# Kernel tuning notes

Hardware: AMD Instinct MI355X
Metric: run time of the kernel (lower is better)

The kernel has to match this reference:

```python
import jax, jax.numpy as jnp
import numpy as np

NUM_STEPS = 64  # num_steps from init
DROP_P = 0.5


def _lstm_cell(x, h, c, W_ih, W_hh, b_ih, b_hh):
    # PyTorch LSTMCell: gates ordered i, f, g, o
    g = x @ W_ih.T + b_ih + h @ W_hh.T + b_hh
    i, f, gg, o = jnp.split(g, 4, axis=-1)
    c2 = jax.nn.sigmoid(f) * c + jax.nn.sigmoid(i) * jnp.tanh(gg)
    h2 = jax.nn.sigmoid(o) * jnp.tanh(c2)
    return h2, c2


def setup_inputs() -> dict:
    key = jax.random.key(0)
    ks = jax.random.split(key, 12)
    s = 0.02
    return {
        "xs": jax.random.normal(ks[0], (128, 128, 512), jnp.float32),
        "W_ih0": jax.random.normal(ks[1], (4096, 512), jnp.float32) * s,
        "W_hh0": jax.random.normal(ks[2], (4096, 1024), jnp.float32) * s,
        "b_ih0": jax.random.normal(ks[3], (4096,), jnp.float32) * s,
        "b_hh0": jax.random.normal(ks[4], (4096,), jnp.float32) * s,
        "W_ih1": jax.random.normal(ks[5], (4096, 1024), jnp.float32) * s,
        "W_hh1": jax.random.normal(ks[6], (4096, 1024), jnp.float32) * s,
        "b_ih1": jax.random.normal(ks[7], (4096,), jnp.float32) * s,
        "b_hh1": jax.random.normal(ks[8], (4096,), jnp.float32) * s,
        "W_cls": jax.random.normal(ks[9], (1000, 1024), jnp.float32) * s,
        "b_cls": jax.random.normal(ks[10], (1000,), jnp.float32) * s,
        "drop_u": jax.random.uniform(ks[11], (128, 1024), jnp.float32),
    }


def reference(xs, W_ih0, W_hh0, b_ih0, b_hh0, W_ih1, W_hh1, b_ih1, b_hh1,
              W_cls, b_cls, drop_u):
    B, T, D = xs.shape
    start = T - NUM_STEPS - 9  # forward reads xs[:, -num_steps-9+t, :]
    seq = jnp.transpose(xs[:, start:start + NUM_STEPS, :], (1, 0, 2))  # [S,B,D]
    H0, H1 = W_hh0.shape[1], W_hh1.shape[1]
    init = (jnp.zeros((B, H0), xs.dtype), jnp.zeros((B, H0), xs.dtype),
            jnp.zeros((B, H1), xs.dtype), jnp.zeros((B, H1), xs.dtype))

    def step(carry, x):
        h0, c0, h1, c1 = carry
        h0, c0 = _lstm_cell(x, h0, c0, W_ih0, W_hh0, b_ih0, b_hh0)
        h1, c1 = _lstm_cell(h0, h1, c1, W_ih1, W_hh1, b_ih1, b_hh1)
        return (h0, c0, h1, c1), None

    (h0, c0, h1, c1), _ = jax.lax.scan(step, init, seq)
    # F.dropout(p=0.5) with a deterministic mask derived from drop_u
    keep = (drop_u > DROP_P).astype(xs.dtype)
    x = h1 * keep / (1.0 - DROP_P)
    return x @ W_cls.T + b_cls
```

## Files before the change

kernel.cpp:

```cpp
#include <hip/hip_runtime.h>
#include <hip/hip_bf16.h>
#include <hip/hip_cooperative_groups.h>


typedef __attribute__((ext_vector_type(8))) short s8v;
typedef __attribute__((ext_vector_type(4))) float f4v;
typedef unsigned short bfu;

#define BATCH 128
#define HID   1024
#define NSTEP 64
#define TDIM  128
#define DDIM  512
#define TSTART 55
#define HSLOT 131072

__device__ __forceinline__ bfu f2bf(float f) {
    union { float f; unsigned int u; } v; v.f = f;
    unsigned int r = (v.u + 0x7FFFu + ((v.u >> 16) & 1u)) >> 16;
    return (bfu)r;
}
__device__ __forceinline__ float sigm(float x) {
    return 1.f / (1.f + __expf(-x));
}

__device__ __forceinline__ void load8_sc(const bfu* p, s8v (&o)[8]) {
    const bfu* p2 = p + 2048;
    asm volatile(
        "global_load_dwordx4 %0, %[a0], off sc0 sc1\n\t"
        "global_load_dwordx4 %1, %[a0], off offset:1024 sc0 sc1\n\t"
        "global_load_dwordx4 %2, %[a0], off offset:2048 sc0 sc1\n\t"
        "global_load_dwordx4 %3, %[a0], off offset:3072 sc0 sc1\n\t"
        "global_load_dwordx4 %4, %[a1], off sc0 sc1\n\t"
        "global_load_dwordx4 %5, %[a1], off offset:1024 sc0 sc1\n\t"
        "global_load_dwordx4 %6, %[a1], off offset:2048 sc0 sc1\n\t"
        "global_load_dwordx4 %7, %[a1], off offset:3072 sc0 sc1\n\t"
        "s_waitcnt vmcnt(0)"
        : "=&v"(o[0]), "=&v"(o[1]), "=&v"(o[2]), "=&v"(o[3]),
          "=&v"(o[4]), "=&v"(o[5]), "=&v"(o[6]), "=&v"(o[7])
        : [a0]"v"(p), [a1]"v"(p2)
        : "memory");
}

__global__ void prep_kernel(
    const float* __restrict__ xs,
    const float* __restrict__ Wih0, const float* __restrict__ Whh0,
    const float* __restrict__ Wih1, const float* __restrict__ Whh1,
    const float* __restrict__ Wcls,
    const float* __restrict__ bih0, const float* __restrict__ bhh0,
    const float* __restrict__ bih1, const float* __restrict__ bhh1,
    bfu* __restrict__ xbf, bfu* __restrict__ wih0b, bfu* __restrict__ whh0b,
    bfu* __restrict__ wih1b, bfu* __restrict__ whh1b, bfu* __restrict__ wclsb,
    float* __restrict__ bias0, float* __restrict__ bias1,
    bfu* __restrict__ h0ring, bfu* __restrict__ h1ring, int* __restrict__ flags)
{
    const size_t NX  = (size_t)NSTEP * BATCH * DDIM;
    const size_t E1  = NX  + (size_t)4096 * 512;
    const size_t E2  = E1  + (size_t)4096 * 1024;
    const size_t E3  = E2  + (size_t)4096 * 1024;
    const size_t E4  = E3  + (size_t)4096 * 1024;
    const size_t E5  = E4  + (size_t)1000 * 1024;
    const size_t E6  = E5  + 4096;
    const size_t E7  = E6  + 4096;
    const size_t E8  = E7  + HSLOT;
    const size_t E9  = E8  + HSLOT;
    const size_t E10 = E9  + 1024;

    size_t stride = (size_t)gridDim.x * blockDim.x;
    for (size_t i = (size_t)blockIdx.x * blockDim.x + threadIdx.x; i < E10; i += stride) {
        if (i < NX) {
            size_t t   = i >> 16;
            int    rem = (int)(i & 65535);
            int chunk = rem >> 9;
            int le    = rem & 511;
            int l = le >> 3, e = le & 7;
            int m  = chunk >> 4;
            int kk = chunk & 15;
            int row = m * 16 + (l & 15);
            int k   = kk * 32 + (l >> 4) * 8 + e;
            xbf[i] = f2bf(xs[(size_t)row * (TDIM * DDIM) + (TSTART + t) * DDIM + k]);
        } else if (i < E1) { size_t j = i - NX;  wih0b[j] = f2bf(Wih0[j]); }
        else if (i < E2)   { size_t j = i - E1;  whh0b[j] = f2bf(Whh0[j]); }
        else if (i < E3)   { size_t j = i - E2;  wih1b[j] = f2bf(Wih1[j]); }
        else if (i < E4)   { size_t j = i - E3;  whh1b[j] = f2bf(Whh1[j]); }
        else if (i < E5)   { size_t j = i - E4;  wclsb[j] = f2bf(Wcls[j]); }
        else if (i < E6)   { size_t j = i - E5;  bias0[j] = bih0[j] + bhh0[j]; }
        else if (i < E7)   { size_t j = i - E6;  bias1[j] = bih1[j] + bhh1[j]; }
        else if (i < E8)   { h0ring[i - E7] = 0; }
        else if (i < E9)   { h1ring[i - E8] = 0; }
        else               { flags[i - E9] = 0; }
    }
}

template<bool SC1, int CH1>
__device__ __forceinline__ void layer_step(
    const bfu* __restrict__ A1, const bfu* __restrict__ A2,
    const bfu* __restrict__ wlds, float (*eps)[33],
    bfu* __restrict__ h_out, float* __restrict__ h_out_f32,
    int tid, int n0, const float (&bg)[8], float& cA, float& cB)
{
    const int l  = tid & 63;
    const int w  = tid >> 6;
    const int lr = l & 15;
    const int kg = l >> 4;

    f4v acc0 = {0.f, 0.f, 0.f, 0.f};
    f4v acc1 = {0.f, 0.f, 0.f, 0.f};

    {
        const bfu* ap  = A1 + (size_t)(w * CH1) * 512 + l * 8;
        const bfu* b0p = wlds + l * 8;
        const bfu* b1p = wlds + (size_t)CH1 * 512 + l * 8;
        if constexpr (SC1) {
            #pragma unroll
            for (int g = 0; g < CH1 / 8; ++g) {
                s8v o[8];
                load8_sc(ap, o); ap += 8 * 512;
                #pragma unroll
                for (int c = 0; c < 8; ++c) {
                    s8v b0 = *(const s8v*)b0p; b0p += 512;
                    s8v b1 = *(const s8v*)b1p; b1p += 512;
                    acc0 = __builtin_amdgcn_mfma_f32_16x16x32_bf16(o[c], b0, acc0, 0, 0, 0);
                    acc1 = __builtin_amdgcn_mfma_f32_16x16x32_bf16(o[c], b1, acc1, 0, 0, 0);
                }
            }
        } else {
            #pragma unroll 8
            for (int kk = 0; kk < CH1; ++kk) {
                s8v a  = *(const s8v*)ap;  ap  += 512;
                s8v b0 = *(const s8v*)b0p; b0p += 512;
                s8v b1 = *(const s8v*)b1p; b1p += 512;
                acc0 = __builtin_amdgcn_mfma_f32_16x16x32_bf16(a, b0, acc0, 0, 0, 0);
                acc1 = __builtin_amdgcn_mfma_f32_16x16x32_bf16(a, b1, acc1, 0, 0, 0);
            }
        }
    }
    {
        const bfu* ap  = A2 + (size_t)(w * 32) * 512 + l * 8;
        const bfu* b0p = wlds + (size_t)(2 * CH1) * 512 + l * 8;
        const bfu* b1p = wlds + (size_t)(2 * CH1 + 32) * 512 + l * 8;
        #pragma unroll
        for (int g = 0; g < 4; ++g) {
            s8v o[8];
            load8_sc(ap, o); ap += 8 * 512;
            #pragma unroll
            for (int c = 0; c < 8; ++c) {
                s8v b0 = *(const s8v*)b0p; b0p += 512;
                s8v b1 = *(const s8v*)b1p; b1p += 512;
                acc0 = __builtin_amdgcn_mfma_f32_16x16x32_bf16(o[c], b0, acc0, 0, 0, 0);
                acc1 = __builtin_amdgcn_mfma_f32_16x16x32_bf16(o[c], b1, acc1, 0, 0, 0);
            }
        }
    }

    {
        const int rbase = w * 16 + kg * 4;
        #pragma unroll
        for (int r = 0; r < 4; ++r) {
            eps[rbase + r][lr]      = acc0[r];
            eps[rbase + r][16 + lr] = acc1[r];
        }
    }
    __syncthreads();

    {
        const int row = tid >> 2;
        const int up  = tid & 3;
        const int e0  = 2 * up;
        const int ne  = n0 + e0;
        float gi0 = eps[row][e0]          + bg[0];
        float gi1 = eps[row][e0 + 1]      + bg[1];
        float gf0 = eps[row][8 + e0]      + bg[2];
        float gf1 = eps[row][8 + e0 + 1]  + bg[3];
        float gg0 = eps[row][16 + e0]     + bg[4];
        float gg1 = eps[row][16 + e0 + 1] + bg[5];
        float go0 = eps[row][24 + e0]     + bg[6];
        float go1 = eps[row][24 + e0 + 1] + bg[7];
        float cn0 = sigm(gf0) * cA + sigm(gi0) * tanhf(gg0);
        float cn1 = sigm(gf1) * cB + sigm(gi1) * tanhf(gg1);
        cA = cn0; cB = cn1;
        float hn0 = sigm(go0) * tanhf(cn0);
        float hn1 = sigm(go1) * tanhf(cn1);
        const int idx = ((row >> 4) * 32 + (ne >> 5)) * 512
                      + (((ne >> 3) & 3) * 16 + (row & 15)) * 8 + (ne & 7);
        unsigned int pk = (unsigned int)f2bf(hn0) | ((unsigned int)f2bf(hn1) << 16);
        __hip_atomic_store((unsigned int*)(h_out + idx), pk,
                           __ATOMIC_RELAXED, __HIP_MEMORY_SCOPE_AGENT);
        if (h_out_f32) {
            h_out_f32[(size_t)row * HID + ne]     = hn0;
            h_out_f32[(size_t)row * HID + ne + 1] = hn1;
        }
    }
    asm volatile("s_waitcnt vmcnt(0)" ::: "memory");
    __syncthreads();
}

__global__ __launch_bounds__(512)
void persist_kernel(
    const bfu* __restrict__ xbf,
    const bfu* __restrict__ wih0, const bfu* __restrict__ whh0,
    const bfu* __restrict__ wih1, const bfu* __restrict__ whh1,
    const float* __restrict__ bias0, const float* __restrict__ bias1,
    bfu* __restrict__ h0ring, bfu* __restrict__ h1ring,
    float* __restrict__ h1f, int* __restrict__ flags)
{
    __shared__ bfu   wlds[65536];
    __shared__ float eps[128][33];

    const int tid  = threadIdx.x;
    const int role = blockIdx.x & 1;
    const int n0   = (blockIdx.x >> 1) * 8;

    int* h0done = flags;
    int* h1done = flags + 64;
    int* h0rel  = flags + 128;

    const bfu*   W1   = role ? wih1 : wih0;
    const bfu*   W2   = role ? whh1 : whh0;
    const float* bias = role ? bias1 : bias0;
    const int    K1   = role ? 1024 : 512;
    const int    CH1  = K1 >> 5;

    {
        const int units = (2 * CH1 + 64) * 64;
        for (int u0 = tid; u0 < units; u0 += 512) {
            const int c = u0 >> 6, l = u0 & 63;
            const int lr = l & 15, kg = l >> 4;
            const bfu* Wsrc; int K, nt, kk;
            if (c < 2 * CH1) { Wsrc = W1; K = K1;   nt = c / CH1; kk = c % CH1; }
            else { const int c2 = c - 2 * CH1; Wsrc = W2; K = 1024; nt = c2 >> 5; kk = c2 & 31; }
            const int cl = nt * 16 + lr;
            const int j  = (cl >> 3) * HID + n0 + (cl & 7);
            s8v v = *(const s8v*)(Wsrc + (size_t)j * K + kk * 32 + kg * 8);
            *(s8v*)(wlds + (size_t)c * 512 + l * 8) = v;
        }
    }
    __syncthreads();

    float bg[8];
    {
        const int ne = n0 + 2 * (tid & 3);
        bg[0] = bias[ne];             bg[1] = bias[ne + 1];
        bg[2] = bias[HID + ne];       bg[3] = bias[HID + ne + 1];
        bg[4] = bias[2 * HID + ne];   bg[5] = bias[2 * HID + ne + 1];
        bg[6] = bias[3 * HID + ne];   bg[7] = bias[3 * HID + ne + 1];
    }
    float cA = 0.f, cB = 0.f;

    if (role == 0) {
        for (int t = 0; t < NSTEP; ++t) {
            if (tid == 0) {
                if (t > 0)
                    while (__hip_atomic_load(&h0done[t - 1], __ATOMIC_RELAXED,
                                             __HIP_MEMORY_SCOPE_AGENT) < 128)
                        __builtin_amdgcn_s_sleep(1);
                if (t >= 16)
                    while (__hip_atomic_load(&h0rel[t - 16], __ATOMIC_RELAXED,
                                             __HIP_MEMORY_SCOPE_AGENT) < 128)
                        __builtin_amdgcn_s_sleep(1);
            }
            __syncthreads();
            const bfu* h0prev = h0ring + (size_t)(t & 15) * HSLOT;
            bfu*       h0cur  = h0ring + (size_t)((t + 1) & 15) * HSLOT;
            layer_step<false, 16>(xbf + (size_t)t * 65536, h0prev, wlds, eps,
                                  h0cur, nullptr, tid, n0, bg, cA, cB);
            if (tid == 0)
                __hip_atomic_fetch_add(&h0done[t], 1, __ATOMIC_RELAXED,
                                       __HIP_MEMORY_SCOPE_AGENT);
        }
    } else {
        for (int t = 0; t < NSTEP; ++t) {
            if (tid == 0) {
                while (__hip_atomic_load(&h0done[t], __ATOMIC_RELAXED,
                                         __HIP_MEMORY_SCOPE_AGENT) < 128)
                    __builtin_amdgcn_s_sleep(1);
                if (t > 0)
                    while (__hip_atomic_load(&h1done[t - 1], __ATOMIC_RELAXED,
                                             __HIP_MEMORY_SCOPE_AGENT) < 128)
                        __builtin_amdgcn_s_sleep(1);
            }
            __syncthreads();
            const bfu* h0t    = h0ring + (size_t)((t + 1) & 15) * HSLOT;
            const bfu* h1prev = h1ring + (size_t)(t & 3) * HSLOT;
            bfu*       h1cur  = h1ring + (size_t)((t + 1) & 3) * HSLOT;
            layer_step<true, 32>(h0t, h1prev, wlds, eps,
                                 h1cur, (t == NSTEP - 1) ? h1f : nullptr,
                                 tid, n0, bg, cA, cB);
            if (tid == 0) {
                __hip_atomic_fetch_add(&h1done[t], 1, __ATOMIC_RELAXED,
                                       __HIP_MEMORY_SCOPE_AGENT);
                __hip_atomic_fetch_add(&h0rel[t], 1, __ATOMIC_RELAXED,
                                       __HIP_MEMORY_SCOPE_AGENT);
            }
        }
    }
}

__global__ __launch_bounds__(512)
void cls_kernel(const float* __restrict__ h1f, const float* __restrict__ du,
                const bfu* __restrict__ Wc, const float* __restrict__ bc,
                float* __restrict__ out)
{
    const int tid = threadIdx.x;
    const int l   = tid & 63;
    const int w   = tid >> 6;
    const int lr  = l & 15;
    const int kg  = l >> 4;
    const int j   = blockIdx.x * 16 + lr;
    const int jW  = (j < 1000) ? j : 999;

    f4v acc = {0.f, 0.f, 0.f, 0.f};
    const float* hp = h1f + (size_t)(w * 16 + lr) * HID + kg * 8;
    const float* dp = du  + (size_t)(w * 16 + lr) * HID + kg * 8;
    const bfu*   bp = Wc  + (size_t)jW * HID + kg * 8;
    #pragma unroll 4
    for (int kk = 0; kk < HID; kk += 32) {
        f4v h0v = *(const f4v*)hp;
        f4v h1v = *(const f4v*)(hp + 4);
        f4v d0v = *(const f4v*)dp;
        f4v d1v = *(const f4v*)(dp + 4);
        s8v a;
        #pragma unroll
        for (int e = 0; e < 4; ++e) {
            a[e]     = (short)f2bf(d0v[e] > 0.5f ? h0v[e] * 2.f : 0.f);
            a[4 + e] = (short)f2bf(d1v[e] > 0.5f ? h1v[e] * 2.f : 0.f);
        }
        s8v b = *(const s8v*)bp;
        acc = __builtin_amdgcn_mfma_f32_16x16x32_bf16(a, b, acc, 0, 0, 0);
        hp += 32; dp += 32; bp += 32;
    }
    if (j < 1000) {
        const float bj = bc[j];
        const int rbase = w * 16 + kg * 4;
        #pragma unroll
        for (int r = 0; r < 4; ++r)
            out[(size_t)(rbase + r) * 1000 + j] = acc[r] + bj;
    }
}

extern "C" void kernel_launch(void* const* d_in, const int* in_sizes, int n_in,
                              void* d_out, int out_size, void* d_ws, size_t ws_size,
                              hipStream_t stream)
{
    const float* xs   = (const float*)d_in[0];
    const float* Wih0 = (const float*)d_in[1];
    const float* Whh0 = (const float*)d_in[2];
    const float* bih0 = (const float*)d_in[3];
    const float* bhh0 = (const float*)d_in[4];
    const float* Wih1 = (const float*)d_in[5];
    const float* Whh1 = (const float*)d_in[6];
    const float* bih1 = (const float*)d_in[7];
    const float* bhh1 = (const float*)d_in[8];
    const float* Wcls = (const float*)d_in[9];
    const float* bcls = (const float*)d_in[10];
    const float* du   = (const float*)d_in[11];
    float* out = (float*)d_out;

    char* p = (char*)d_ws;
    auto alloc = [&](size_t bytes) {
        char* r = p; p += (bytes + 255) & ~(size_t)255; return r;
    };
    bfu*   xbf   = (bfu*)  alloc((size_t)NSTEP * BATCH * DDIM * 2);
    bfu*   wih0b = (bfu*)  alloc((size_t)4096 * 512 * 2);
    bfu*   whh0b = (bfu*)  alloc((size_t)4096 * 1024 * 2);
    bfu*   wih1b = (bfu*)  alloc((size_t)4096 * 1024 * 2);
    bfu*   whh1b = (bfu*)  alloc((size_t)4096 * 1024 * 2);
    bfu*   wclsb = (bfu*)  alloc((size_t)1000 * 1024 * 2);
    float* bias0 = (float*)alloc(4096 * 4);
    float* bias1 = (float*)alloc(4096 * 4);
    bfu*   h0ring = (bfu*) alloc((size_t)16 * HSLOT * 2);
    bfu*   h1ring = (bfu*) alloc((size_t)4 * HSLOT * 2);
    float* h1f    = (float*)alloc((size_t)BATCH * HID * 4);
    int*   flags  = (int*) alloc(1024 * 4);
    (void)ws_size; (void)in_sizes; (void)n_in; (void)out_size;

    prep_kernel<<<2048, 256, 0, stream>>>(
        xs, Wih0, Whh0, Wih1, Whh1, Wcls, bih0, bhh0, bih1, bhh1,
        xbf, wih0b, whh0b, wih1b, whh1b, wclsb, bias0, bias1,
        h0ring, h1ring, flags);

    {
        void* args[] = {
            (void*)&xbf, (void*)&wih0b, (void*)&whh0b, (void*)&wih1b,
            (void*)&whh1b, (void*)&bias0, (void*)&bias1,
            (void*)&h0ring, (void*)&h1ring, (void*)&h1f, (void*)&flags
        };
        hipLaunchCooperativeKernel((const void*)persist_kernel,
                                   dim3(256), dim3(512), args, 0, stream);
    }

    cls_kernel<<<63, 512, 0, stream>>>(h1f, du, wclsb, bcls, out);
}
```

Measured before the change: 827.4 us.

## Split LSTM persistent kernel into four GEMM roles with partial-sum handoff

Splits each LSTM layer's work across four block roles: the input projection for layer 0, the recurrent projection for layer 0, the input projection for layer 1, and the recurrent projection for layer 1. The input-projection roles write fp32 partial gate sums that the recurrent roles add before the LSTM epilogue. This takes the input GEMMs off the serial recurrence path and lets them run ahead. It also moves from 16x16x32 to 32x32x16 MFMA tiles with a matching xbf and weight layout, shrinks the h0 ring, and replaces the cooperative launch with a plain launch. The cost is extra global partial-sum traffic and many more flag spin-waits. It also depends on all 256 blocks being co-resident without the cooperative-launch guarantee.

```diff
diff --git a/kernel.cpp b/kernel.cpp
--- a/kernel.cpp
+++ b/kernel.cpp
@@ -1,10 +1,10 @@
 #include <hip/hip_runtime.h>
 #include <hip/hip_bf16.h>
-#include <hip/hip_cooperative_groups.h>
-
-
-typedef __attribute__((ext_vector_type(8))) short s8v;
-typedef __attribute__((ext_vector_type(4))) float f4v;
+
+
+typedef __attribute__((ext_vector_type(8)))  short s8v;
+typedef __attribute__((ext_vector_type(4)))  float f4v;
+typedef __attribute__((ext_vector_type(16))) float f16v;
 typedef unsigned short bfu;
 
 #define BATCH 128
@@ -15,6 +15,13 @@
 #define TSTART 55
 #define HSLOT 131072
 
+#define F_H0D(t)  ((t) * 16)
+#define F_H1D(t)  (1024 + (t) * 16)
+#define F_PCN(t)  (2048 + (t) * 16)
+#define F_XD(t,i) (3072 + (t) * 64 + (i))
+#define F_PD(t,i) (7168 + (t) * 64 + (i))
+#define NFLAGS    11264
+
 __device__ __forceinline__ bfu f2bf(float f) {
     union { float f; unsigned int u; } v; v.f = f;
     unsigned int r = (v.u + 0x7FFFu + ((v.u >> 16) & 1u)) >> 16;
@@ -22,6 +29,12 @@
 }
 __device__ __forceinline__ float sigm(float x) {
     return 1.f / (1.f + __expf(-x));
+}
+__device__ __forceinline__ f16v zero16() {
+    f16v a;
+    #pragma unroll
+    for (int r = 0; r < 16; ++r) a[r] = 0.f;
+    return a;
 }
 
 __device__ __forceinline__ void load8_sc(const bfu* p, s8v (&o)[8]) {
@@ -42,6 +55,35 @@
         : "memory");
 }
 
+__device__ __forceinline__ void store16_sc(float* p, const f16v& a) {
+    f4v v0 = {a[0], a[1], a[2], a[3]},   v1 = {a[4], a[5], a[6], a[7]};
+    f4v v2 = {a[8], a[9], a[10], a[11]}, v3 = {a[12], a[13], a[14], a[15]};
+    asm volatile(
+        "global_store_dwordx4 %0, %1, off sc0 sc1\n\t"
+        "global_store_dwordx4 %0, %2, off offset:16 sc0 sc1\n\t"
+        "global_store_dwordx4 %0, %3, off offset:32 sc0 sc1\n\t"
+        "global_store_dwordx4 %0, %4, off offset:48 sc0 sc1"
+        :: "v"(p), "v"(v0), "v"(v1), "v"(v2), "v"(v3)
+        : "memory");
+}
+
+__device__ __forceinline__ void addpart_sc(const float* p, f16v& acc) {
+    f4v v0, v1, v2, v3;
+    asm volatile(
+        "global_load_dwordx4 %0, %[ad], off sc0 sc1\n\t"
+        "global_load_dwordx4 %1, %[ad], off offset:16 sc0 sc1\n\t"
+        "global_load_dwordx4 %2, %[ad], off offset:32 sc0 sc1\n\t"
+        "global_load_dwordx4 %3, %[ad], off offset:48 sc0 sc1\n\t"
+        "s_waitcnt vmcnt(0)"
+        : "=&v"(v0), "=&v"(v1), "=&v"(v2), "=&v"(v3)
+        : [ad]"v"(p) : "memory");
+    #pragma unroll
+    for (int r = 0; r < 4; ++r) {
+        acc[r] += v0[r]; acc[4 + r] += v1[r];
+        acc[8 + r] += v2[r]; acc[12 + r] += v3[r];
+    }
+}
+
 __global__ void prep_kernel(
     const float* __restrict__ xs,
     const float* __restrict__ Wih0, const float* __restrict__ Whh0,
@@ -64,7 +106,7 @@
     const size_t E7  = E6  + 4096;
     const size_t E8  = E7  + HSLOT;
     const size_t E9  = E8  + HSLOT;
-    const size_t E10 = E9  + 1024;
+    const size_t E10 = E9  + NFLAGS;
 
     size_t stride = (size_t)gridDim.x * blockDim.x;
     for (size_t i = (size_t)blockIdx.x * blockDim.x + threadIdx.x; i < E10; i += stride) {
@@ -72,12 +114,11 @@
             size_t t   = i >> 16;
             int    rem = (int)(i & 65535);
             int chunk = rem >> 9;
-            int le    = rem & 511;
-            int l = le >> 3, e = le & 7;
-            int m  = chunk >> 4;
-            int kk = chunk & 15;
-            int row = m * 16 + (l & 15);
-            int k   = kk * 32 + (l >> 4) * 8 + e;
+            int l = (rem >> 3) & 63, e = rem & 7;
+            int m  = chunk >> 5;
+            int ks = chunk & 31;
+            int row = m * 32 + (l & 31);
+            int k   = ks * 16 + (l >> 5) * 8 + e;
             xbf[i] = f2bf(xs[(size_t)row * (TDIM * DDIM) + (TSTART + t) * DDIM + k]);
         } else if (i < E1) { size_t j = i - NX;  wih0b[j] = f2bf(Wih0[j]); }
         else if (i < E2)   { size_t j = i - E1;  whh0b[j] = f2bf(Whh0[j]); }
@@ -92,106 +133,85 @@
     }
 }
 
-template<bool SC1, int CH1>
-__device__ __forceinline__ void layer_step(
-    const bfu* __restrict__ A1, const bfu* __restrict__ A2,
-    const bfu* __restrict__ wlds, float (*eps)[33],
-    bfu* __restrict__ h_out, float* __restrict__ h_out_f32,
-    int tid, int n0, const float (&bg)[8], float& cA, float& cB)
-{
-    const int l  = tid & 63;
-    const int w  = tid >> 6;
-    const int lr = l & 15;
-    const int kg = l >> 4;
-
-    f4v acc0 = {0.f, 0.f, 0.f, 0.f};
-    f4v acc1 = {0.f, 0.f, 0.f, 0.f};
-
-    {
-        const bfu* ap  = A1 + (size_t)(w * CH1) * 512 + l * 8;
-        const bfu* b0p = wlds + l * 8;
-        const bfu* b1p = wlds + (size_t)CH1 * 512 + l * 8;
-        if constexpr (SC1) {
+template<bool SC, int KS>
+__device__ __forceinline__ void gemm32(const bfu* __restrict__ Abase,
+                                       const bfu* __restrict__ bbase,
+                                       f16v& acc, int m, int l)
+{
+    const bfu* ap = Abase + (size_t)(m * KS) * 512 + l * 8;
+    const bfu* bp = bbase + l * 8;
+    #pragma unroll
+    for (int g = 0; g < KS / 8; ++g) {
+        s8v o[8];
+        if constexpr (SC) {
+            load8_sc(ap, o);
+        } else {
             #pragma unroll
-            for (int g = 0; g < CH1 / 8; ++g) {
-                s8v o[8];
-                load8_sc(ap, o); ap += 8 * 512;
-                #pragma unroll
-                for (int c = 0; c < 8; ++c) {
-                    s8v b0 = *(const s8v*)b0p; b0p += 512;
-                    s8v b1 = *(const s8v*)b1p; b1p += 512;
-                    acc0 = __builtin_amdgcn_mfma_f32_16x16x32_bf16(o[c], b0, acc0, 0, 0, 0);
-                    acc1 = __builtin_amdgcn_mfma_f32_16x16x32_bf16(o[c], b1, acc1, 0, 0, 0);
-                }
+            for (int c = 0; c < 8; ++c) o[c] = *(const s8v*)(ap + c * 512);
+        }
+        ap += 8 * 512;
+        #pragma unroll
+        for (int c = 0; c < 8; ++c) {
+            s8v b = *(const s8v*)bp; bp += 512;
+            acc = __builtin_amdgcn_mfma_f32_32x32x16_bf16(o[c], b, acc, 0, 0, 0);
+        }
+    }
+}
+
+__device__ __forceinline__ void lstm_epi32(
+    f16v& acc, float (*eps)[66], int tid, int n0,
+    const float* bgq, float* cst, bfu* __restrict__ h_out,
+    float* __restrict__ h1f_opt)
+{
+    const int l = tid & 63, w = tid >> 6;
+    const int m = w >> 1, nt = w & 1, hi = l >> 5, cc = l & 31;
+    const int row64 = tid >> 3, up = tid & 7;
+    const int u0 = 2 * up;
+    const int cb = ((u0 >> 3) * 32) + (u0 & 7);
+    const int k = n0 + u0;
+
+    #pragma unroll
+    for (int h = 0; h < 2; ++h) {
+        if ((m >> 1) == h) {
+            #pragma unroll
+            for (int r = 0; r < 16; ++r)
+                eps[(m & 1) * 32 + (r & 3) + 8 * (r >> 2) + 4 * hi][nt * 32 + cc] = acc[r];
+        }
+        __syncthreads();
+        {
+            const int row = h * 64 + row64;
+            float gi0 = eps[row64][cb]      + bgq[0];
+            float gi1 = eps[row64][cb + 1]  + bgq[1];
+            float gf0 = eps[row64][cb + 8]  + bgq[2];
+            float gf1 = eps[row64][cb + 9]  + bgq[3];
+            float gg0 = eps[row64][cb + 16] + bgq[4];
+            float gg1 = eps[row64][cb + 17] + bgq[5];
+            float go0 = eps[row64][cb + 24] + bgq[6];
+            float go1 = eps[row64][cb + 25] + bgq[7];
+            float cn0 = sigm(gf0) * cst[h * 2]     + sigm(gi0) * tanhf(gg0);
+            float cn1 = sigm(gf1) * cst[h * 2 + 1] + sigm(gi1) * tanhf(gg1);
+            cst[h * 2] = cn0; cst[h * 2 + 1] = cn1;
+            float hn0 = sigm(go0) * tanhf(cn0);
+            float hn1 = sigm(go1) * tanhf(cn1);
+            const int chunk = (row >> 5) * 64 + (k >> 4);
+            const int lp = ((k >> 3) & 1) * 32 + (row & 31);
+            const int elem = chunk * 512 + lp * 8 + (k & 7);
+            unsigned int pk = (unsigned int)f2bf(hn0) | ((unsigned int)f2bf(hn1) << 16);
+            __hip_atomic_store((unsigned int*)(h_out + elem), pk,
+                               __ATOMIC_RELAXED, __HIP_MEMORY_SCOPE_AGENT);
+            if (h1f_opt) {
+                h1f_opt[(size_t)row * HID + k]     = hn0;
+                h1f_opt[(size_t)row * HID + k + 1] = hn1;
             }
-        } else {
-            #pragma unroll 8
-            for (int kk = 0; kk < CH1; ++kk) {
-                s8v a  = *(const s8v*)ap;  ap  += 512;
-                s8v b0 = *(const s8v*)b0p; b0p += 512;
-                s8v b1 = *(const s8v*)b1p; b1p += 512;
-                acc0 = __builtin_amdgcn_mfma_f32_16x16x32_bf16(a, b0, acc0, 0, 0, 0);
-                acc1 = __builtin_amdgcn_mfma_f32_16x16x32_bf16(a, b1, acc1, 0, 0, 0);
-            }
-        }
-    }
-    {
-        const bfu* ap  = A2 + (size_t)(w * 32) * 512 + l * 8;
-        const bfu* b0p = wlds + (size_t)(2 * CH1) * 512 + l * 8;
-        const bfu* b1p = wlds + (size_t)(2 * CH1 + 32) * 512 + l * 8;
-        #pragma unroll
-        for (int g = 0; g < 4; ++g) {
-            s8v o[8];
-            load8_sc(ap, o); ap += 8 * 512;
-            #pragma unroll
-            for (int c = 0; c < 8; ++c) {
-                s8v b0 = *(const s8v*)b0p; b0p += 512;
-                s8v b1 = *(const s8v*)b1p; b1p += 512;
-                acc0 = __builtin_amdgcn_mfma_f32_16x16x32_bf16(o[c], b0, acc0, 0, 0, 0);
-                acc1 = __builtin_amdgcn_mfma_f32_16x16x32_bf16(o[c], b1, acc1, 0, 0, 0);
-            }
-        }
-    }
-
-    {
-        const int rbase = w * 16 + kg * 4;
-        #pragma unroll
-        for (int r = 0; r < 4; ++r) {
-            eps[rbase + r][lr]      = acc0[r];
-            eps[rbase + r][16 + lr] = acc1[r];
-        }
-    }
-    __syncthreads();
-
-    {
-        const int row = tid >> 2;
-        const int up  = tid & 3;
-        const int e0  = 2 * up;
-        const int ne  = n0 + e0;
-        float gi0 = eps[row][e0]          + bg[0];
-        float gi1 = eps[row][e0 + 1]      + bg[1];
-        float gf0 = eps[row][8 + e0]      + bg[2];
-        float gf1 = eps[row][8 + e0 + 1]  + bg[3];
-        float gg0 = eps[row][16 + e0]     + bg[4];
-        float gg1 = eps[row][16 + e0 + 1] + bg[5];
-        float go0 = eps[row][24 + e0]     + bg[6];
-        float go1 = eps[row][24 + e0 + 1] + bg[7];
-        float cn0 = sigm(gf0) * cA + sigm(gi0) * tanhf(gg0);
-        float cn1 = sigm(gf1) * cB + sigm(gi1) * tanhf(gg1);
-        cA = cn0; cB = cn1;
-        float hn0 = sigm(go0) * tanhf(cn0);
-        float hn1 = sigm(go1) * tanhf(cn1);
-        const int idx = ((row >> 4) * 32 + (ne >> 5)) * 512
-                      + (((ne >> 3) & 3) * 16 + (row & 15)) * 8 + (ne & 7);
-        unsigned int pk = (unsigned int)f2bf(hn0) | ((unsigned int)f2bf(hn1) << 16);
-        __hip_atomic_store((unsigned int*)(h_out + idx), pk,
-                           __ATOMIC_RELAXED, __HIP_MEMORY_SCOPE_AGENT);
-        if (h_out_f32) {
-            h_out_f32[(size_t)row * HID + ne]     = hn0;
-            h_out_f32[(size_t)row * HID + ne + 1] = hn1;
-        }
-    }
-    asm volatile("s_waitcnt vmcnt(0)" ::: "memory");
+        }
+        __syncthreads();
+    }
+}
+
+__device__ __forceinline__ void waitflag(int* p, int target, int tid) {
+    if (tid == 0)
+        while (__hip_atomic_load(p, __ATOMIC_RELAXED, __HIP_MEMORY_SCOPE_AGENT) < target)
+            __builtin_amdgcn_s_sleep(1);
     __syncthreads();
 }
 
@@ -202,96 +222,104 @@
     const bfu* __restrict__ wih1, const bfu* __restrict__ whh1,
     const float* __restrict__ bias0, const float* __restrict__ bias1,
     bfu* __restrict__ h0ring, bfu* __restrict__ h1ring,
-    float* __restrict__ h1f, int* __restrict__ flags)
+    float* __restrict__ xpart, float* __restrict__ ppart,
+    float* __restrict__ h1f, int* __restrict__ F)
 {
     __shared__ bfu   wlds[65536];
-    __shared__ float eps[128][33];
+    __shared__ float eps[64][66];
 
     const int tid  = threadIdx.x;
-    const int role = blockIdx.x & 1;
-    const int n0   = (blockIdx.x >> 1) * 8;
-
-    int* h0done = flags;
-    int* h1done = flags + 64;
-    int* h0rel  = flags + 128;
-
-    const bfu*   W1   = role ? wih1 : wih0;
-    const bfu*   W2   = role ? whh1 : whh0;
-    const float* bias = role ? bias1 : bias0;
-    const int    K1   = role ? 1024 : 512;
-    const int    CH1  = K1 >> 5;
-
-    {
-        const int units = (2 * CH1 + 64) * 64;
-        for (int u0 = tid; u0 < units; u0 += 512) {
-            const int c = u0 >> 6, l = u0 & 63;
-            const int lr = l & 15, kg = l >> 4;
-            const bfu* Wsrc; int K, nt, kk;
-            if (c < 2 * CH1) { Wsrc = W1; K = K1;   nt = c / CH1; kk = c % CH1; }
-            else { const int c2 = c - 2 * CH1; Wsrc = W2; K = 1024; nt = c2 >> 5; kk = c2 & 31; }
-            const int cl = nt * 16 + lr;
-            const int j  = (cl >> 3) * HID + n0 + (cl & 7);
-            s8v v = *(const s8v*)(Wsrc + (size_t)j * K + kk * 32 + kg * 8);
-            *(s8v*)(wlds + (size_t)c * 512 + l * 8) = v;
-        }
+    const int role = blockIdx.x & 3;
+    const int i    = blockIdx.x >> 2;
+    const int n0   = i * 16;
+    const int l = tid & 63, w = tid >> 6;
+    const int m = w >> 1, nt = w & 1;
+
+    const bfu* Wsrc; const float* bias = nullptr; int K;
+    if      (role == 0) { Wsrc = wih0; K = 512; }
+    else if (role == 1) { Wsrc = whh0; K = 1024; bias = bias0; }
+    else if (role == 2) { Wsrc = wih1; K = 1024; }
+    else                { Wsrc = whh1; K = 1024; bias = bias1; }
+    const int KSr = K >> 4;
+    const int ksh = (K == 512) ? 5 : 6;
+
+    for (int u = tid; u < 2 * KSr * 64; u += 512) {
+        int c = u >> 6, ll = u & 63;
+        int ntc = c >> ksh, ks = c & (KSr - 1);
+        int j  = ((ll >> 3) & 3) * 1024 + n0 + ntc * 8 + (ll & 7);
+        int k0 = ks * 16 + (ll >> 5) * 8;
+        *(s8v*)(wlds + (size_t)c * 512 + ll * 8) = *(const s8v*)(Wsrc + (size_t)j * K + k0);
     }
     __syncthreads();
 
-    float bg[8];
-    {
-        const int ne = n0 + 2 * (tid & 3);
-        bg[0] = bias[ne];             bg[1] = bias[ne + 1];
-        bg[2] = bias[HID + ne];       bg[3] = bias[HID + ne + 1];
-        bg[4] = bias[2 * HID + ne];   bg[5] = bias[2 * HID + ne + 1];
-        bg[6] = bias[3 * HID + ne];   bg[7] = bias[3 * HID + ne + 1];
-    }
-    float cA = 0.f, cB = 0.f;
+    float bgq[8] = {0.f, 0.f, 0.f, 0.f, 0.f, 0.f, 0.f, 0.f};
+    float cst[4] = {0.f, 0.f, 0.f, 0.f};
+    if (bias) {
+        const int u0 = 2 * (tid & 7);
+        #pragma unroll
+        for (int g = 0; g < 4; ++g) {
+            bgq[g * 2]     = bias[g * HID + n0 + u0];
+            bgq[g * 2 + 1] = bias[g * HID + n0 + u0 + 1];
+        }
+    }
+
+    const bfu* bnt512 = wlds + (size_t)nt * 32 * 512;
+    const bfu* bnt    = wlds + (size_t)nt * 64 * 512;
 
     if (role == 0) {
         for (int t = 0; t < NSTEP; ++t) {
+            if (t >= 2) waitflag(&F[F_H0D(t - 2)], 64, tid);
+            f16v acc = zero16();
+            gemm32<false, 32>(xbf + (size_t)t * 65536, bnt512, acc, m, l);
+            store16_sc(xpart + ((size_t)((t & 1) * 64 + i)) * 8192 + (w * 64 + l) * 16, acc);
+            asm volatile("s_waitcnt vmcnt(0)" ::: "memory");
+            __syncthreads();
+            if (tid == 0)
+                __hip_atomic_store(&F[F_XD(t, i)], 1, __ATOMIC_RELAXED, __HIP_MEMORY_SCOPE_AGENT);
+        }
+    } else if (role == 1) {
+        for (int t = 0; t < NSTEP; ++t) {
+            if (t >= 1) waitflag(&F[F_H0D(t - 1)], 64, tid);
+            if (t >= 3) waitflag(&F[F_PCN(t - 3)], 64, tid);
+            f16v acc = zero16();
+            gemm32<true, 64>(h0ring + (size_t)(t & 3) * HSLOT, bnt, acc, m, l);
+            waitflag(&F[F_XD(t, i)], 1, tid);
+            addpart_sc(xpart + ((size_t)((t & 1) * 64 + i)) * 8192 + (w * 64 + l) * 16, acc);
+            lstm_epi32(acc, eps, tid, n0, bgq, cst,
+                       h0ring + (size_t)((t + 1) & 3) * HSLOT, nullptr);
+            asm volatile("s_waitcnt vmcnt(0)" ::: "memory");
+            __syncthreads();
+            if (tid == 0)
+                __hip_atomic_fetch_add(&F[F_H0D(t)], 1, __ATOMIC_RELAXED, __HIP_MEMORY_SCOPE_AGENT);
+        }
+    } else if (role == 2) {
+        for (int t = 0; t < NSTEP; ++t) {
+            waitflag(&F[F_H0D(t)], 64, tid);
+            if (t >= 2) waitflag(&F[F_H1D(t - 2)], 64, tid);
+            f16v acc = zero16();
+            gemm32<true, 64>(h0ring + (size_t)((t + 1) & 3) * HSLOT, bnt, acc, m, l);
+            store16_sc(ppart + ((size_t)((t & 1) * 64 + i)) * 8192 + (w * 64 + l) * 16, acc);
+            asm volatile("s_waitcnt vmcnt(0)" ::: "memory");
+            __syncthreads();
             if (tid == 0) {
-                if (t > 0)
-                    while (__hip_atomic_load(&h0done[t - 1], __ATOMIC_RELAXED,
-                                             __HIP_MEMORY_SCOPE_AGENT) < 128)
-                        __builtin_amdgcn_s_sleep(1);
-                if (t >= 16)
-                    while (__hip_atomic_load(&h0rel[t - 16], __ATOMIC_RELAXED,
-                                             __HIP_MEMORY_SCOPE_AGENT) < 128)
-                        __builtin_amdgcn_s_sleep(1);
+                __hip_atomic_store(&F[F_PD(t, i)], 1, __ATOMIC_RELAXED, __HIP_MEMORY_SCOPE_AGENT);
+                __hip_atomic_fetch_add(&F[F_PCN(t)], 1, __ATOMIC_RELAXED, __HIP_MEMORY_SCOPE_AGENT);
             }
-            __syncthreads();
-            const bfu* h0prev = h0ring + (size_t)(t & 15) * HSLOT;
-            bfu*       h0cur  = h0ring + (size_t)((t + 1) & 15) * HSLOT;
-            layer_step<false, 16>(xbf + (size_t)t * 65536, h0prev, wlds, eps,
-                                  h0cur, nullptr, tid, n0, bg, cA, cB);
-            if (tid == 0)
-                __hip_atomic_fetch_add(&h0done[t], 1, __ATOMIC_RELAXED,
-                                       __HIP_MEMORY_SCOPE_AGENT);
         }
     } else {
         for (int t = 0; t < NSTEP; ++t) {
-            if (tid == 0) {
-                while (__hip_atomic_load(&h0done[t], __ATOMIC_RELAXED,
-                                         __HIP_MEMORY_SCOPE_AGENT) < 128)
-                    __builtin_amdgcn_s_sleep(1);
-                if (t > 0)
-                    while (__hip_atomic_load(&h1done[t - 1], __ATOMIC_RELAXED,
-                                             __HIP_MEMORY_SCOPE_AGENT) < 128)
-                        __builtin_amdgcn_s_sleep(1);
-            }
+            if (t >= 1) waitflag(&F[F_H1D(t - 1)], 64, tid);
+            f16v acc = zero16();
+            gemm32<true, 64>(h1ring + (size_t)(t & 3) * HSLOT, bnt, acc, m, l);
+            waitflag(&F[F_PD(t, i)], 1, tid);
+            addpart_sc(ppart + ((size_t)((t & 1) * 64 + i)) * 8192 + (w * 64 + l) * 16, acc);
+            lstm_epi32(acc, eps, tid, n0, bgq, cst,
+                       h1ring + (size_t)((t + 1) & 3) * HSLOT,
+                       (t == NSTEP - 1) ? h1f : nullptr);
+            asm volatile("s_waitcnt vmcnt(0)" ::: "memory");
             __syncthreads();
-            const bfu* h0t    = h0ring + (size_t)((t + 1) & 15) * HSLOT;
-            const bfu* h1prev = h1ring + (size_t)(t & 3) * HSLOT;
-            bfu*       h1cur  = h1ring + (size_t)((t + 1) & 3) * HSLOT;
-            layer_step<true, 32>(h0t, h1prev, wlds, eps,
-                                 h1cur, (t == NSTEP - 1) ? h1f : nullptr,
-                                 tid, n0, bg, cA, cB);
-            if (tid == 0) {
-                __hip_atomic_fetch_add(&h1done[t], 1, __ATOMIC_RELAXED,
-                                       __HIP_MEMORY_SCOPE_AGENT);
-                __hip_atomic_fetch_add(&h0rel[t], 1, __ATOMIC_RELAXED,
-                                       __HIP_MEMORY_SCOPE_AGENT);
-            }
+            if (tid == 0)
+                __hip_atomic_fetch_add(&F[F_H1D(t)], 1, __ATOMIC_RELAXED, __HIP_MEMORY_SCOPE_AGENT);
         }
     }
 }
@@ -360,18 +388,20 @@
     auto alloc = [&](size_t bytes) {
         char* r = p; p += (bytes + 255) & ~(size_t)255; return r;
     };
-    bfu*   xbf   = (bfu*)  alloc((size_t)NSTEP * BATCH * DDIM * 2);
-    bfu*   wih0b = (bfu*)  alloc((size_t)4096 * 512 * 2);
-    bfu*   whh0b = (bfu*)  alloc((size_t)4096 * 1024 * 2);
-    bfu*   wih1b = (bfu*)  alloc((size_t)4096 * 1024 * 2);
-    bfu*   whh1b = (bfu*)  alloc((size_t)4096 * 1024 * 2);
-    bfu*   wclsb = (bfu*)  alloc((size_t)1000 * 1024 * 2);
-    float* bias0 = (float*)alloc(4096 * 4);
-    float* bias1 = (float*)alloc(4096 * 4);
-    bfu*   h0ring = (bfu*) alloc((size_t)16 * HSLOT * 2);
-    bfu*   h1ring = (bfu*) alloc((size_t)4 * HSLOT * 2);
+    bfu*   xbf    = (bfu*)  alloc((size_t)NSTEP * BATCH * DDIM * 2);
+    bfu*   wih0b  = (bfu*)  alloc((size_t)4096 * 512 * 2);
+    bfu*   whh0b  = (bfu*)  alloc((size_t)4096 * 1024 * 2);
+    bfu*   wih1b  = (bfu*)  alloc((size_t)4096 * 1024 * 2);
+    bfu*   whh1b  = (bfu*)  alloc((size_t)4096 * 1024 * 2);
+    bfu*   wclsb  = (bfu*)  alloc((size_t)1000 * 1024 * 2);
+    float* bias0  = (float*)alloc(4096 * 4);
+    float* bias1  = (float*)alloc(4096 * 4);
+    bfu*   h0ring = (bfu*)  alloc((size_t)4 * HSLOT * 2);
+    bfu*   h1ring = (bfu*)  alloc((size_t)4 * HSLOT * 2);
+    float* xpart  = (float*)alloc((size_t)2 * 64 * 8192 * 4);
+    float* ppart  = (float*)alloc((size_t)2 * 64 * 8192 * 4);
     float* h1f    = (float*)alloc((size_t)BATCH * HID * 4);
-    int*   flags  = (int*) alloc(1024 * 4);
+    int*   flags  = (int*)  alloc((size_t)NFLAGS * 4);
     (void)ws_size; (void)in_sizes; (void)n_in; (void)out_size;
 
     prep_kernel<<<2048, 256, 0, stream>>>(
@@ -379,15 +409,9 @@
         xbf, wih0b, whh0b, wih1b, whh1b, wclsb, bias0, bias1,
         h0ring, h1ring, flags);
 
-    {
-        void* args[] = {
-            (void*)&xbf, (void*)&wih0b, (void*)&whh0b, (void*)&wih1b,
-            (void*)&whh1b, (void*)&bias0, (void*)&bias1,
-            (void*)&h0ring, (void*)&h1ring, (void*)&h1f, (void*)&flags
-        };
-        hipLaunchCooperativeKernel((const void*)persist_kernel,
-                                   dim3(256), dim3(512), args, 0, stream);
-    }
+    persist_kernel<<<256, 512, 0, stream>>>(
+        xbf, wih0b, whh0b, wih1b, whh1b, bias0, bias1,
+        h0ring, h1ring, xpart, ppart, h1f, flags);
 
     cls_kernel<<<63, 512, 0, stream>>>(h1f, du, wclsb, bcls, out);
 }
```

Result: slower. 967.1 us (+16.9%).
